# Optimization experiments

Hardware: AMD Instinct MI355X
Metric: run time of the kernel (lower is better)

Reference implementation:

```python
import jax, jax.numpy as jnp
import numpy as np

TAU = 2.0      # LIF membrane time constant
V_TH = 1.0     # spike threshold, v_reset = 0 (hard reset)
ALPHA = 2.0    # ATan surrogate alpha (spikingjelly default)
EPS = 1e-5     # BatchNorm eps

B, L, C = 32, 512, 256
T = 4          # num_steps
HID = 1024
LAYERS = 2
K = 3          # conv kernel width


@jax.custom_vjp
def spike_fn(x):
    # heaviside forward, ATan surrogate backward
    return (x >= 0.0).astype(x.dtype)

def _spike_fwd(x):
    return spike_fn(x), x

def _spike_bwd(x, g):
    return (g * (ALPHA / 2.0) / (1.0 + (jnp.pi / 2.0 * ALPHA * x) ** 2),)

spike_fn.defvjp(_spike_fwd, _spike_bwd)


def lif(x_seq):
    """Multi-step LIF (decay_input=True, hard reset to 0, detach_reset=True).
    x_seq: [T, ...] -> spikes [T, ...]."""
    def step(v, x):
        v = v + (x - v) / TAU
        s = spike_fn(v - V_TH)
        v = v * (1.0 - jax.lax.stop_gradient(s))  # detach_reset
        return v, s
    _, spikes = jax.lax.scan(step, jnp.zeros_like(x_seq[0]), x_seq)
    return spikes


def setup_inputs() -> dict:
    key = jax.random.key(0)
    ks = jax.random.split(key, 8)
    def sc(fan_in):
        return 1.0 / np.sqrt(fan_in)
    return {
        "inputs": jax.random.normal(ks[0], (B, L, C), jnp.float32),
        "conv_w": jax.random.normal(ks[1], (T, 1, 1, K), jnp.float32) * sc(K),
        "conv_b": jnp.zeros((T,), jnp.float32),
        "bn_gamma": jnp.ones((T,), jnp.float32),
        "bn_beta": jnp.zeros((T,), jnp.float32),
        "bn_mean": jnp.zeros((T,), jnp.float32),
        "bn_var": jnp.ones((T,), jnp.float32),
        "enc_w": jax.random.normal(ks[2], (HID, C), jnp.float32) * sc(C),
        "enc_b": jnp.zeros((HID,), jnp.float32),
        "cell_w": jax.random.normal(ks[3], (LAYERS, HID, HID), jnp.float32) * sc(HID),
        "cell_b": jnp.zeros((LAYERS, HID), jnp.float32),
    }


def reference(inputs, conv_w, conv_b, bn_gamma, bn_beta, bn_mean, bn_var,
              enc_w, enc_b, cell_w, cell_b):
    # ---- ConvEncoder ----
    # [B,L,C] -> [B,1,C,L]
    x = inputs.transpose(0, 2, 1)[:, None, :, :]
    y = jax.lax.conv_general_dilated(
        x, conv_w, window_strides=(1, 1),
        padding=((0, 0), (K // 2, K // 2)),
        dimension_numbers=("NCHW", "OIHW", "NCHW"))
    y = y + conv_b[None, :, None, None]          # [B,T,C,L]
    # BatchNorm2d over T channels (eval mode with running stats)
    inv = bn_gamma / jnp.sqrt(bn_var + EPS)
    y = (y - bn_mean[None, :, None, None]) * inv[None, :, None, None] \
        + bn_beta[None, :, None, None]
    y = y.transpose(1, 0, 2, 3)                  # [T,B,C,L]
    spks = lif(y)                                # [T,B,C,L]
    # ---- SpikeRNN trunk ----
    h = spks.transpose(0, 1, 3, 2)               # [T,B,L,C]
    h = jnp.einsum("tblc,dc->tbld", h, enc_w) + enc_b
    h = lif(h)                                   # init_lif
    for i in range(LAYERS):                      # SpikeRNNCells
        h = jnp.einsum("tbld,ed->tble", h, cell_w[i]) + cell_b[i]
        h = lif(h)
    out = h.mean(axis=0)                         # [B,L,HID]
    return out, out.mean(axis=1)                 # ([B,L,HID], [B,HID])
```

## Files before the change

### kernel.cpp

```cpp
#include <hip/hip_runtime.h>
#include <hip/hip_bf16.h>
#include <stdint.h>

#define Bb 32
#define Lx 512
#define Cc 256
#define Tt 4
#define HID 1024
#define RR (Bb*Lx)
#define MRf (RR*Tt)

typedef int i32x4 __attribute__((ext_vector_type(4)));

__device__ __forceinline__ void gl16(const void* g, void* l) {
    __builtin_amdgcn_global_load_lds(
        (const __attribute__((address_space(1))) unsigned int*)g,
        (__attribute__((address_space(3))) unsigned int*)l, 16, 0, 0);
}
__device__ __forceinline__ void blockbar() {
    asm volatile("" ::: "memory");
    __builtin_amdgcn_s_barrier();
    asm volatile("" ::: "memory");
}

__global__ void zero_f(float* p, int n) {
    if ((int)threadIdx.x < n) p[threadIdx.x] = 0.0f;
}
__global__ void absmax3(const float* __restrict__ enc_w, const float* __restrict__ cell_w,
                        float* __restrict__ out) {
    const int y = blockIdx.y;
    const int n = (y == 0) ? HID*Cc : HID*HID;
    const float* w = (y == 0) ? enc_w : cell_w + (size_t)(y-1)*HID*HID;
    float v = 0.0f;
    for (int i = blockIdx.x*256 + threadIdx.x; i < n; i += gridDim.x*256)
        v = fmaxf(v, fabsf(w[i]));
    #pragma unroll
    for (int o = 32; o; o >>= 1) v = fmaxf(v, __shfl_down(v, o));
    if ((threadIdx.x & 63) == 0)
        atomicMax((unsigned*)(out + y), __float_as_uint(v));
}
__global__ void quant3(const float* __restrict__ enc_w, const float* __restrict__ cell_w,
                       const float* __restrict__ amax,
                       int8_t* __restrict__ qEnc, int8_t* __restrict__ qC0,
                       int8_t* __restrict__ qC1, float* __restrict__ invOut) {
    const int y = blockIdx.y;
    const int n = (y == 0) ? HID*Cc : HID*HID;
    const float* w = (y == 0) ? enc_w : cell_w + (size_t)(y-1)*HID*HID;
    int8_t* q = (y == 0) ? qEnc : (y == 1 ? qC0 : qC1);
    float m = fmaxf(amax[y], 1e-20f);
    float e = floorf(log2f(126.0f * 16384.0f / m));
    float sp = exp2f(e);
    if (m * sp > 126.0f * 16384.0f) sp *= 0.5f;
    if (blockIdx.x == 0 && threadIdx.x == 0) invOut[y] = 1.0f / sp;
    int i = blockIdx.x*256 + threadIdx.x;
    if (i >= n) return;
    float v  = rintf(w[i] * sp);
    float i1 = rintf(v * (1.0f/16384.0f));
    float r1 = v - i1 * 16384.0f;
    float i2 = rintf(r1 * (1.0f/128.0f));
    float r2 = r1 - i2 * 128.0f;
    q[i]               = (int8_t)i1;
    q[(size_t)n + i]   = (int8_t)i2;
    q[(size_t)2*n + i] = (int8_t)r2;
}

__global__ void conv_bn_lif(const float* __restrict__ x,
                            const float* __restrict__ cw, const float* __restrict__ cb,
                            const float* __restrict__ g,  const float* __restrict__ be,
                            const float* __restrict__ mu, const float* __restrict__ var,
                            int8_t* __restrict__ spk) {
    int idx = blockIdx.x * blockDim.x + threadIdx.x;
    if (idx >= Bb*Lx*Cc/4) return;
    int bl = idx / (Cc/4);
    int c4 = (idx % (Cc/4)) * 4;
    int l  = bl % Lx;
    float4 x0 = *(const float4*)(x + (size_t)bl*Cc + c4);
    float4 xm = (l > 0)    ? *(const float4*)(x + (size_t)bl*Cc + c4 - Cc) : float4{0,0,0,0};
    float4 xp = (l < Lx-1) ? *(const float4*)(x + (size_t)bl*Cc + c4 + Cc) : float4{0,0,0,0};
    float v0=0, v1=0, v2=0, v3=0;
    #pragma unroll
    for (int t = 0; t < Tt; ++t) {
        float w0 = cw[t*3+0], w1 = cw[t*3+1], w2 = cw[t*3+2];
        float inv = g[t] / sqrtf(var[t] + 1e-5f);
        float off = (cb[t] - mu[t]) * inv + be[t];
        float y0 = (w0*xm.x + w1*x0.x + w2*xp.x) * inv + off;
        float y1 = (w0*xm.y + w1*x0.y + w2*xp.y) * inv + off;
        float y2 = (w0*xm.z + w1*x0.z + w2*xp.z) * inv + off;
        float y3 = (w0*xm.w + w1*x0.w + w2*xp.w) * inv + off;
        v0 = v0 + (y0 - v0)*0.5f;  v1 = v1 + (y1 - v1)*0.5f;
        v2 = v2 + (y2 - v2)*0.5f;  v3 = v3 + (y3 - v3)*0.5f;
        float s0 = (v0 >= 1.0f) ? 1.0f : 0.0f;  float s1 = (v1 >= 1.0f) ? 1.0f : 0.0f;
        float s2 = (v2 >= 1.0f) ? 1.0f : 0.0f;  float s3 = (v3 >= 1.0f) ? 1.0f : 0.0f;
        uchar4 pk = { (uint8_t)s0, (uint8_t)s1, (uint8_t)s2, (uint8_t)s3 };
        *(uchar4*)(spk + (size_t)(bl*4 + t)*Cc + c4) = pk;
        v0 *= (1.0f - s0);  v1 *= (1.0f - s1);  v2 *= (1.0f - s2);  v3 *= (1.0f - s3);
    }
}

template<int K, bool FINAL>
__global__ __launch_bounds__(512, 2)
void gemm_lif(const int8_t* __restrict__ A,
              const int8_t* __restrict__ Wq,
              const float* __restrict__ invs,
              const float* __restrict__ bias,
              int8_t* __restrict__ spk_out, float* __restrict__ out_mean) {
    constexpr int KT  = K / 64;
    constexpr int NKT = 3 * KT;
    __shared__ int8_t lds[4 * 32768];

    const int tid  = threadIdx.x;
    const int lane = tid & 63;
    const int wid  = tid >> 6;
    const int wm   = wid >> 2;
    const int wn   = wid & 3;
    const int bid  = blockIdx.x;
    const int idx_ = bid >> 3;
    const int n0   = (idx_ & 3) * 256;
    const int m0   = ((bid & 7) * 32 + (idx_ >> 2)) * 256;
    const int fr   = lane & 15;
    const int lq   = lane >> 4;
    const int swq  = (lq ^ ((fr >> 1) & 3)) * 16;
    const int srow = tid >> 2;
    const int sl   = (tid & 3) ^ ((srow >> 1) & 3);

    i32x4 acc[8][4] = {};

    auto stage = [&](int t, int8_t* buf) {
        const int8_t* Wc = Wq + (size_t)(t / KT) * HID * K;
        const int ko = (t % KT) * 64;
        gl16(A  + (size_t)(m0 +       srow) * K + ko + sl*16, buf +         tid*16);
        gl16(A  + (size_t)(m0 + 128 + srow) * K + ko + sl*16, buf +  8192 + tid*16);
        gl16(Wc + (size_t)(n0 +       srow) * K + ko + sl*16, buf + 16384 + tid*16);
        gl16(Wc + (size_t)(n0 + 128 + srow) * K + ko + sl*16, buf + 24576 + tid*16);
    };

    stage(0, &lds[0]);
    stage(1, &lds[32768]);
    stage(2, &lds[65536]);

    #pragma unroll 1
    for (int kt = 0; kt < NKT; ++kt) {
        if (kt == KT || kt == 2*KT) {
            #pragma unroll
            for (int i = 0; i < 8; ++i)
                #pragma unroll
                for (int j = 0; j < 4; ++j)
                    acc[i][j] *= 128;
        }
        if (kt < NKT-2)       asm volatile("s_waitcnt vmcnt(8)" ::: "memory");
        else if (kt == NKT-2) asm volatile("s_waitcnt vmcnt(4)" ::: "memory");
        else                  asm volatile("s_waitcnt vmcnt(0)" ::: "memory");
        blockbar();

        const int cb = (kt & 3) * 32768;

        i32x4 af[8], bf[4];
        #pragma unroll
        for (int i = 0; i < 8; ++i)
            af[i] = *(const i32x4*)&lds[cb + (wm*128 + i*16 + fr)*64 + swq];
        #pragma unroll
        for (int j = 0; j < 4; ++j)
            bf[j] = *(const i32x4*)&lds[cb + 16384 + (wn*64 + j*16 + fr)*64 + swq];

        if (kt + 3 < NKT) stage(kt + 3, &lds[((kt + 3) & 3) * 32768]);

        __builtin_amdgcn_s_setprio(1);
        #pragma unroll
        for (int i = 0; i < 8; ++i)
            #pragma unroll
            for (int j = 0; j < 4; ++j)
                acc[i][j] = __builtin_amdgcn_mfma_i32_16x16x64_i8(af[i], bf[j], acc[i][j], 0, 0, 0);
        __builtin_amdgcn_s_setprio(0);
    }

    const float inv = invs[0];
    float bs[4];
    #pragma unroll
    for (int j = 0; j < 4; ++j)
        bs[j] = bias[n0 + wn*64 + j*16 + fr];
    const int rowq = lq * 4;
    #pragma unroll
    for (int i = 0; i < 8; ++i) {
        int rowLocal = m0 + wm*128 + i*16 + rowq;
        int r = rowLocal >> 2;
        #pragma unroll
        for (int j = 0; j < 4; ++j) {
            int n = n0 + wn*64 + j*16 + fr;
            float v = 0.0f, ssum = 0.0f;
            #pragma unroll
            for (int t = 0; t < 4; ++t) {
                float xv = (float)acc[i][j][t] * inv + bs[j];
                v = v + (xv - v) * 0.5f;
                float s = (v >= 1.0f) ? 1.0f : 0.0f;
                if constexpr (FINAL) ssum += s;
                else spk_out[(size_t)(rowLocal + t) * HID + n] = (int8_t)s;
                v = v * (1.0f - s);
            }
            if constexpr (FINAL) out_mean[(size_t)r * HID + n] = ssum * 0.25f;
        }
    }
}

__global__ void mean_partial(const float* __restrict__ out1, float* __restrict__ part) {
    int idx = blockIdx.x * blockDim.x + threadIdx.x;
    if (idx >= 8*Bb*HID) return;
    int seg = idx >> 15;
    int bd  = idx & (Bb*HID - 1);
    int b = bd >> 10, d = bd & (HID-1);
    const float* p = out1 + ((size_t)b*Lx + seg*64)*HID + d;
    float s = 0.0f;
    #pragma unroll 4
    for (int l = 0; l < 64; ++l) s += p[(size_t)l*HID];
    part[idx] = s;
}
__global__ void mean_final(const float* __restrict__ part, float* __restrict__ out2) {
    int idx = blockIdx.x * blockDim.x + threadIdx.x;
    if (idx >= Bb*HID) return;
    float s = 0.0f;
    #pragma unroll
    for (int k = 0; k < 8; ++k) s += part[k*Bb*HID + idx];
    out2[idx] = s * (1.0f / Lx);
}

extern "C" void kernel_launch(void* const* d_in, const int* in_sizes, int n_in,
                              void* d_out, int out_size, void* d_ws, size_t ws_size,
                              hipStream_t stream) {
    const float* x      = (const float*)d_in[0];
    const float* cw     = (const float*)d_in[1];
    const float* cb     = (const float*)d_in[2];
    const float* g      = (const float*)d_in[3];
    const float* be     = (const float*)d_in[4];
    const float* mu     = (const float*)d_in[5];
    const float* var    = (const float*)d_in[6];
    const float* enc_w  = (const float*)d_in[7];
    const float* enc_b  = (const float*)d_in[8];
    const float* cell_w = (const float*)d_in[9];
    const float* cell_b = (const float*)d_in[10];

    float* out1 = (float*)d_out;
    float* out2 = out1 + (size_t)RR * HID;

    uint8_t* ws = (uint8_t*)d_ws;
    int8_t* X = (int8_t*)ws;
    int8_t* Y = (int8_t*)(ws + (size_t)64*1024*1024);
    int8_t* qEnc = (int8_t*)(ws + (size_t)128*1024*1024);
    int8_t* qC0  = qEnc + (size_t)3*HID*Cc;
    int8_t* qC1  = qC0  + (size_t)3*HID*HID;
    float*  amax = (float*)(qC1 + (size_t)3*HID*HID);
    float*  invv = amax + 4;
    float*  part = invv + 4;

    zero_f<<<1, 4, 0, stream>>>(amax, 3);
    absmax3<<<dim3(64, 3), 256, 0, stream>>>(enc_w, cell_w, amax);
    quant3<<<dim3((HID*HID + 255)/256, 3), 256, 0, stream>>>(enc_w, cell_w, amax,
                                                             qEnc, qC0, qC1, invv);

    conv_bn_lif<<<(Bb*Lx*Cc/4 + 255)/256, 256, 0, stream>>>(x, cw, cb, g, be, mu, var, X);

    gemm_lif<Cc,  false><<<1024, 512, 0, stream>>>(X, qEnc, invv + 0, enc_b,      Y, nullptr);
    gemm_lif<HID, false><<<1024, 512, 0, stream>>>(Y, qC0,  invv + 1, cell_b,     X, nullptr);
    gemm_lif<HID, true ><<<1024, 512, 0, stream>>>(X, qC1,  invv + 2, cell_b+HID, nullptr, out1);

    mean_partial<<<(8*Bb*HID + 255)/256, 256, 0, stream>>>(out1, part);
    mean_final<<<(Bb*HID + 255)/256, 256, 0, stream>>>(part, out2);
}
```

Baseline: 449.0 us.

## Quantize weights per row in one kernel and fuse mean into final GEMM

Replaces the global absmax plus quantize kernel pair with a single per-row quantization kernel that computes a per-output-channel scale, and the GEMM epilogue now reads per-column inverse scales. The final GEMM accumulates spike sums per column and atomically adds the L-mean into out2, removing the two mean-reduction kernels and the re-read of out1. This cuts kernel launches and a large memory pass, at the cost of float atomics (order-dependent summation) and a zero-init kernel.

Result: faster. 418.3 us (median of 2 runs) (-6.8%).

```diff
diff --git a/kernel.cpp b/kernel.cpp
--- a/kernel.cpp
+++ b/kernel.cpp
@@ -23,45 +23,43 @@
     asm volatile("" ::: "memory");
 }
 
-__global__ void zero_f(float* p, int n) {
-    if ((int)threadIdx.x < n) p[threadIdx.x] = 0.0f;
-}
-__global__ void absmax3(const float* __restrict__ enc_w, const float* __restrict__ cell_w,
-                        float* __restrict__ out) {
-    const int y = blockIdx.y;
-    const int n = (y == 0) ? HID*Cc : HID*HID;
-    const float* w = (y == 0) ? enc_w : cell_w + (size_t)(y-1)*HID*HID;
-    float v = 0.0f;
-    for (int i = blockIdx.x*256 + threadIdx.x; i < n; i += gridDim.x*256)
-        v = fmaxf(v, fabsf(w[i]));
-    #pragma unroll
-    for (int o = 32; o; o >>= 1) v = fmaxf(v, __shfl_down(v, o));
-    if ((threadIdx.x & 63) == 0)
-        atomicMax((unsigned*)(out + y), __float_as_uint(v));
-}
-__global__ void quant3(const float* __restrict__ enc_w, const float* __restrict__ cell_w,
-                       const float* __restrict__ amax,
-                       int8_t* __restrict__ qEnc, int8_t* __restrict__ qC0,
-                       int8_t* __restrict__ qC1, float* __restrict__ invOut) {
-    const int y = blockIdx.y;
-    const int n = (y == 0) ? HID*Cc : HID*HID;
-    const float* w = (y == 0) ? enc_w : cell_w + (size_t)(y-1)*HID*HID;
-    int8_t* q = (y == 0) ? qEnc : (y == 1 ? qC0 : qC1);
-    float m = fmaxf(amax[y], 1e-20f);
-    float e = floorf(log2f(126.0f * 16384.0f / m));
-    float sp = exp2f(e);
+__global__ void quant_rows(const float* __restrict__ enc_w,
+                           const float* __restrict__ cell_w,
+                           int8_t* __restrict__ qEnc, int8_t* __restrict__ qC0,
+                           int8_t* __restrict__ qC1, float* __restrict__ invN) {
+    const int gw   = (blockIdx.x * blockDim.x + threadIdx.x) >> 6;
+    const int lane = threadIdx.x & 63;
+    const int mat  = gw >> 10;
+    const int row  = gw & 1023;
+    const int Kk   = (mat == 0) ? Cc : HID;
+    const float* w = (mat == 0) ? enc_w + (size_t)row * Cc
+                                : cell_w + (size_t)(mat-1)*HID*HID + (size_t)row * HID;
+    int8_t* q = ((mat == 0) ? qEnc : (mat == 1 ? qC0 : qC1)) + (size_t)row * Kk;
+    const size_t nElem = (size_t)HID * Kk;
+
+    float m = 0.0f;
+    for (int k = lane; k < Kk; k += 64) m = fmaxf(m, fabsf(w[k]));
+    #pragma unroll
+    for (int o = 32; o; o >>= 1) m = fmaxf(m, __shfl_xor(m, o));
+    m = fmaxf(m, 1e-20f);
+    float sp = exp2f(floorf(log2f(126.0f * 16384.0f / m)));
     if (m * sp > 126.0f * 16384.0f) sp *= 0.5f;
-    if (blockIdx.x == 0 && threadIdx.x == 0) invOut[y] = 1.0f / sp;
-    int i = blockIdx.x*256 + threadIdx.x;
-    if (i >= n) return;
-    float v  = rintf(w[i] * sp);
-    float i1 = rintf(v * (1.0f/16384.0f));
-    float r1 = v - i1 * 16384.0f;
-    float i2 = rintf(r1 * (1.0f/128.0f));
-    float r2 = r1 - i2 * 128.0f;
-    q[i]               = (int8_t)i1;
-    q[(size_t)n + i]   = (int8_t)i2;
-    q[(size_t)2*n + i] = (int8_t)r2;
+    if (lane == 0) invN[mat*HID + row] = 1.0f / sp;
+    for (int k = lane; k < Kk; k += 64) {
+        float v  = rintf(w[k] * sp);
+        float i1 = rintf(v * (1.0f/16384.0f));
+        float r1 = v - i1 * 16384.0f;
+        float i2 = rintf(r1 * (1.0f/128.0f));
+        float r2 = r1 - i2 * 128.0f;
+        q[k]           = (int8_t)i1;
+        q[nElem + k]   = (int8_t)i2;
+        q[2*nElem + k] = (int8_t)r2;
+    }
+}
+
+__global__ void zero_out(float* p, int n) {
+    int i = blockIdx.x * 256 + threadIdx.x;
+    if (i < n) p[i] = 0.0f;
 }
 
 __global__ void conv_bn_lif(const float* __restrict__ x,
@@ -101,9 +99,10 @@
 __global__ __launch_bounds__(512, 2)
 void gemm_lif(const int8_t* __restrict__ A,
               const int8_t* __restrict__ Wq,
-              const float* __restrict__ invs,
+              const float* __restrict__ invN,
               const float* __restrict__ bias,
-              int8_t* __restrict__ spk_out, float* __restrict__ out_mean) {
+              int8_t* __restrict__ spk_out, float* __restrict__ out_mean,
+              float* __restrict__ out_sum) {
     constexpr int KT  = K / 64;
     constexpr int NKT = 3 * KT;
     __shared__ int8_t lds[4 * 32768];
@@ -173,11 +172,13 @@
         __builtin_amdgcn_s_setprio(0);
     }
 
-    const float inv = invs[0];
-    float bs[4];
-    #pragma unroll
-    for (int j = 0; j < 4; ++j)
-        bs[j] = bias[n0 + wn*64 + j*16 + fr];
+    float bs[4], iv[4], msum[4] = {0,0,0,0};
+    #pragma unroll
+    for (int j = 0; j < 4; ++j) {
+        int n = n0 + wn*64 + j*16 + fr;
+        bs[j] = bias[n];
+        iv[j] = invN[n];
+    }
     const int rowq = lq * 4;
     #pragma unroll
     for (int i = 0; i < 8; ++i) {
@@ -189,37 +190,32 @@
             float v = 0.0f, ssum = 0.0f;
             #pragma unroll
             for (int t = 0; t < 4; ++t) {
-                float xv = (float)acc[i][j][t] * inv + bs[j];
+                float xv = (float)acc[i][j][t] * iv[j] + bs[j];
                 v = v + (xv - v) * 0.5f;
                 float s = (v >= 1.0f) ? 1.0f : 0.0f;
                 if constexpr (FINAL) ssum += s;
                 else spk_out[(size_t)(rowLocal + t) * HID + n] = (int8_t)s;
                 v = v * (1.0f - s);
             }
-            if constexpr (FINAL) out_mean[(size_t)r * HID + n] = ssum * 0.25f;
+            if constexpr (FINAL) {
+                out_mean[(size_t)r * HID + n] = ssum * 0.25f;
+                msum[j] += ssum;
+            }
         }
     }
-}
-
-__global__ void mean_partial(const float* __restrict__ out1, float* __restrict__ part) {
-    int idx = blockIdx.x * blockDim.x + threadIdx.x;
-    if (idx >= 8*Bb*HID) return;
-    int seg = idx >> 15;
-    int bd  = idx & (Bb*HID - 1);
-    int b = bd >> 10, d = bd & (HID-1);
-    const float* p = out1 + ((size_t)b*Lx + seg*64)*HID + d;
-    float s = 0.0f;
-    #pragma unroll 4
-    for (int l = 0; l < 64; ++l) s += p[(size_t)l*HID];
-    part[idx] = s;
-}
-__global__ void mean_final(const float* __restrict__ part, float* __restrict__ out2) {
-    int idx = blockIdx.x * blockDim.x + threadIdx.x;
-    if (idx >= Bb*HID) return;
-    float s = 0.0f;
-    #pragma unroll
-    for (int k = 0; k < 8; ++k) s += part[k*Bb*HID + idx];
-    out2[idx] = s * (1.0f / Lx);
+    if constexpr (FINAL) {
+        const int b = m0 >> 11;
+        #pragma unroll
+        for (int j = 0; j < 4; ++j) {
+            float v = msum[j];
+            v += __shfl_xor(v, 16);
+            v += __shfl_xor(v, 32);
+            if (lq == 0) {
+                int n = n0 + wn*64 + j*16 + fr;
+                atomicAdd(out_sum + (size_t)b * HID + n, v * (0.25f / 512.0f));
+            }
+        }
+    }
 }
 
 extern "C" void kernel_launch(void* const* d_in, const int* in_sizes, int n_in,
@@ -246,21 +242,17 @@
     int8_t* qEnc = (int8_t*)(ws + (size_t)128*1024*1024);
     int8_t* qC0  = qEnc + (size_t)3*HID*Cc;
     int8_t* qC1  = qC0  + (size_t)3*HID*HID;
-    float*  amax = (float*)(qC1 + (size_t)3*HID*HID);
-    float*  invv = amax + 4;
-    float*  part = invv + 4;
-
-    zero_f<<<1, 4, 0, stream>>>(amax, 3);
-    absmax3<<<dim3(64, 3), 256, 0, stream>>>(enc_w, cell_w, amax);
-    quant3<<<dim3((HID*HID + 255)/256, 3), 256, 0, stream>>>(enc_w, cell_w, amax,
-                                                             qEnc, qC0, qC1, invv);
+    float*  invN = (float*)(qC1 + (size_t)3*HID*HID);
+
+    quant_rows<<<768, 256, 0, stream>>>(enc_w, cell_w, qEnc, qC0, qC1, invN);
 
     conv_bn_lif<<<(Bb*Lx*Cc/4 + 255)/256, 256, 0, stream>>>(x, cw, cb, g, be, mu, var, X);
-
-    gemm_lif<Cc,  false><<<1024, 512, 0, stream>>>(X, qEnc, invv + 0, enc_b,      Y, nullptr);
-    gemm_lif<HID, false><<<1024, 512, 0, stream>>>(Y, qC0,  invv + 1, cell_b,     X, nullptr);
-    gemm_lif<HID, true ><<<1024, 512, 0, stream>>>(X, qC1,  invv + 2, cell_b+HID, nullptr, out1);
-
-    mean_partial<<<(8*Bb*HID + 255)/256, 256, 0, stream>>>(out1, part);
-    mean_final<<<(Bb*HID + 255)/256, 256, 0, stream>>>(part, out2);
-}
+    zero_out<<<(Bb*HID + 255)/256, 256, 0, stream>>>(out2, Bb*HID);
+
+    gemm_lif<Cc,  false><<<1024, 512, 0, stream>>>(X, qEnc, invN,        enc_b,
+                                                   Y, nullptr, nullptr);
+    gemm_lif<HID, false><<<1024, 512, 0, stream>>>(Y, qC0,  invN + HID,  cell_b,
+                                                   X, nullptr, nullptr);
+    gemm_lif<HID, true ><<<1024, 512, 0, stream>>>(X, qC1,  invN + 2*HID, cell_b + HID,
+                                                   nullptr, out1, out2);
+}
```
